# Kernel tuning notes

Measured on AMD Instinct MI355X. Metric: run time of the kernel, lower is better.

## Reference

```python
import jax, jax.numpy as jnp
import numpy as np

N_QUBITS = 8
TRASH = 1
DEPTH = 2
DIM = 2 ** N_QUBITS  # 256

# Qiskit little-endian: amplitude index k has qubit 0 as LSB. Reshaping a
# 256-vector to (2,)*8 puts qubit (N-1-a) on tensor axis a (axis 0 = MSB).
# Observable j is SparsePauliOp with 'Z' at string pos j => Z on qubit N-1-j
# => tensor axis j. So exp_j = sum probs * (1 - 2*bit_axis_j).


def _rx(t):
    c = jnp.cos(t / 2).astype(jnp.complex64)
    ms = (-1j * jnp.sin(t / 2)).astype(jnp.complex64)
    return jnp.stack([jnp.stack([c, ms]), jnp.stack([ms, c])])


def _ry(t):
    c = jnp.cos(t / 2).astype(jnp.complex64)
    s = jnp.sin(t / 2).astype(jnp.complex64)
    return jnp.stack([jnp.stack([c, -s]), jnp.stack([s, c])])


def _rz(t):
    e = jnp.exp((-0.5j) * t.astype(jnp.complex64))
    z = jnp.zeros_like(e)
    return jnp.stack([jnp.stack([e, z]), jnp.stack([z, jnp.conj(e)])])


def _apply_1q(psi, U, q):
    ax = 1 + (N_QUBITS - 1 - q)
    return jnp.moveaxis(jnp.tensordot(psi, U, axes=([ax], [1])), -1, ax)


def _apply_cx(psi, c, t):
    axc = 1 + (N_QUBITS - 1 - c)
    axt = 1 + (N_QUBITS - 1 - t)
    shape = [1] * psi.ndim
    shape[axc] = 2
    ctrl = (jnp.arange(2).reshape(shape) == 1)
    return jnp.where(ctrl, jnp.flip(psi, axis=axt), psi)


def _r3_ansatz(psi, theta, nq, depth):
    k = 0
    for _ in range(depth):
        for q in range(nq):
            psi = _apply_1q(psi, _rx(theta[k + 0]), q)
            psi = _apply_1q(psi, _ry(theta[k + 1]), q)
            psi = _apply_1q(psi, _rz(theta[k + 2]), q)
            k += 3
        for q in range(nq - 1):  # linear entanglement
            psi = _apply_cx(psi, q, q + 1)
    return psi


# sign matrix for Z expectations: S[j, k] = 1 - 2*bit_{N-1-j}(k)
_k = np.arange(DIM)
_SIGNS = np.stack([1.0 - 2.0 * ((_k >> (N_QUBITS - 1 - j)) & 1)
                   for j in range(N_QUBITS)]).astype(np.float32)  # (8, 256)


def setup_inputs() -> dict:
    key = jax.random.key(0)
    k1, k2, k3, k4 = jax.random.split(key, 4)
    return {
        "x": jax.random.normal(k1, (32, 1024, 256), dtype=jnp.float32),
        "theta1": jax.random.normal(k2, (DEPTH * N_QUBITS * 3,), dtype=jnp.float32),
        "theta2": jax.random.normal(k3, (DEPTH * (N_QUBITS - TRASH) * 3,), dtype=jnp.float32),
        "theta3": jax.random.normal(k4, (DEPTH * N_QUBITS * 3,), dtype=jnp.float32),
    }


def reference(x, theta1, theta2, theta3):
    B, T, D = x.shape
    xf = x.reshape(B * T, D)
    # amplitude encode: normalize classical vector into quantum amplitudes
    norm = jnp.linalg.norm(xf, axis=1, keepdims=True)
    norm = jnp.where(norm == 0, jnp.float32(1e-8), norm)
    psi = (xf / norm).astype(jnp.complex64).reshape((B * T,) + (2,) * N_QUBITS)
    # ansatz: U1 (8q) -> U2 (7q) -> U3 (8q)
    psi = _r3_ansatz(psi, theta1, N_QUBITS, DEPTH)
    psi = _r3_ansatz(psi, theta2, N_QUBITS - TRASH, DEPTH)
    psi = _r3_ansatz(psi, theta3, N_QUBITS, DEPTH)
    # Z expectation on each observable
    probs = (jnp.abs(psi) ** 2).reshape(B * T, DIM)
    y = probs @ jnp.asarray(_SIGNS).T  # (B*T, 8)
    # amplitude decode: normalize, |.|^2, zero-pad to DIM
    yn = jnp.linalg.norm(y, axis=1, keepdims=True)
    yn = jnp.where(yn == 0, jnp.float32(1e-8), yn)
    cv = (y / yn) ** 2
    out = jnp.pad(cv, ((0, 0), (0, DIM - N_QUBITS)))
    return out.reshape(B, T, DIM)
```

## Files before the change

kernel.cpp:

```cpp
#include <hip/hip_runtime.h>
#include <math.h>


#define DEV __device__ __forceinline__

typedef __attribute__((ext_vector_type(8))) short short8;
typedef __attribute__((ext_vector_type(4))) float f32x4;

DEV float2 cmul(float2 a, float2 b) {
  return make_float2(a.x * b.x - a.y * b.y, a.x * b.y + a.y * b.x);
}
DEV float2 cadd(float2 a, float2 b) { return make_float2(a.x + b.x, a.y + b.y); }

DEV unsigned short bf_rne(float v) {
  unsigned u = __float_as_uint(v);
  return (unsigned short)((u + 0x7FFFu + ((u >> 16) & 1u)) >> 16);
}

template <int CTRL>
DEV float dppf(float v) {
  return __int_as_float(__builtin_amdgcn_mov_dpp(__float_as_int(v), CTRL, 0xF, 0xF, true));
}
DEV float px1(float v) { return dppf<0xB1>(v); }
DEV float px2(float v) { return dppf<0x4E>(v); }
DEV float px4(float v) { return dppf<0x1B>(dppf<0x141>(v)); }
DEV float px8(float v) { return dppf<0x141>(dppf<0x140>(v)); }
DEV float fsgn(float v, int m) { return __int_as_float(__float_as_int(v) ^ m); }


struct Psi4 { float re[4]; float im[4]; };

template <int Q>
DEV void pair_gate(Psi4& s, const float2* __restrict__ Mlo,
                   const float2* __restrict__ Mhi, int lane) {
  const int b0 = (lane >> Q) & 1, b1 = (lane >> (Q + 1)) & 1;
  float2 lo_d = Mlo[b0 * 2 + b0];
  float2 lo_o = Mlo[b0 * 2 + (b0 ^ 1)];
  float2 hi_d = Mhi[b1 * 2 + b1];
  float2 hi_o = Mhi[b1 * 2 + (b1 ^ 1)];
  float2 c00 = cmul(hi_d, lo_d);
  float2 c01 = cmul(hi_d, lo_o);
  float2 c10 = cmul(hi_o, lo_d);
  float2 c11 = cmul(hi_o, lo_o);
  const int m0 = 1 << Q, m1 = 2 << Q;
#pragma unroll
  for (int r = 0; r < 4; ++r) {
    float ar = s.re[r], ai = s.im[r];
    float p0r = __shfl_xor(ar, m0, 64), p0i = __shfl_xor(ai, m0, 64);
    float p1r = __shfl_xor(ar, m1, 64), p1i = __shfl_xor(ai, m1, 64);
    float p2r = __shfl_xor(ar, m0 | m1, 64), p2i = __shfl_xor(ai, m0 | m1, 64);
    float nr = c00.x * ar - c00.y * ai + c01.x * p0r - c01.y * p0i
             + c10.x * p1r - c10.y * p1i + c11.x * p2r - c11.y * p2i;
    float ni = c00.x * ai + c00.y * ar + c01.x * p0i + c01.y * p0r
             + c10.x * p1i + c10.y * p1r + c11.x * p2i + c11.y * p2r;
    s.re[r] = nr; s.im[r] = ni;
  }
}

DEV void regpair_gate(Psi4& s, const float2* __restrict__ Mlo,
                      const float2* __restrict__ Mhi) {
  float nr[4], ni[4];
#pragma unroll
  for (int r = 0; r < 4; ++r) {
    const int b0 = r & 1, b1 = (r >> 1) & 1;
    float2 c00 = cmul(Mhi[b1 * 2 + b1], Mlo[b0 * 2 + b0]);
    float2 c01 = cmul(Mhi[b1 * 2 + b1], Mlo[b0 * 2 + (b0 ^ 1)]);
    float2 c10 = cmul(Mhi[b1 * 2 + (b1 ^ 1)], Mlo[b0 * 2 + b0]);
    float2 c11 = cmul(Mhi[b1 * 2 + (b1 ^ 1)], Mlo[b0 * 2 + (b0 ^ 1)]);
    nr[r] = c00.x * s.re[r] - c00.y * s.im[r]
          + c01.x * s.re[r ^ 1] - c01.y * s.im[r ^ 1]
          + c10.x * s.re[r ^ 2] - c10.y * s.im[r ^ 2]
          + c11.x * s.re[r ^ 3] - c11.y * s.im[r ^ 3];
    ni[r] = c00.x * s.im[r] + c00.y * s.re[r]
          + c01.x * s.im[r ^ 1] + c01.y * s.re[r ^ 1]
          + c10.x * s.im[r ^ 2] + c10.y * s.re[r ^ 2]
          + c11.x * s.im[r ^ 3] + c11.y * s.re[r ^ 3];
  }
#pragma unroll
  for (int r = 0; r < 4; ++r) { s.re[r] = nr[r]; s.im[r] = ni[r]; }
}

DEV void reg0_gate(Psi4& s, const float2* __restrict__ M) {
  float nr[4], ni[4];
#pragma unroll
  for (int r = 0; r < 4; ++r) {
    const int b = r & 1;
    float2 d = M[b * 2 + b], o = M[b * 2 + (b ^ 1)];
    nr[r] = d.x * s.re[r] - d.y * s.im[r] + o.x * s.re[r ^ 1] - o.y * s.im[r ^ 1];
    ni[r] = d.x * s.im[r] + d.y * s.re[r] + o.x * s.im[r ^ 1] + o.y * s.re[r ^ 1];
  }
#pragma unroll
  for (int r = 0; r < 4; ++r) { s.re[r] = nr[r]; s.im[r] = ni[r]; }
}

template <bool FULL8>
DEV void perm_cx(Psi4& s, int lane) {
  const int slane = (lane ^ (lane << 1)) & 63;
  const bool L5 = ((lane >> 5) & 1) != 0;
  float nr[4], ni[4];
#pragma unroll
  for (int r = 0; r < 4; ++r) {
    const int r0 = r & 1, r1 = (r >> 1) & 1;
    const int hiBit = FULL8 ? (r1 ^ r0) : r1;
    const int sA = (hiBit << 1) | r0;
    const int sB = sA ^ 1;
    float aRe = __shfl(s.re[sA], slane, 64);
    float aIm = __shfl(s.im[sA], slane, 64);
    float bRe = __shfl(s.re[sB], slane, 64);
    float bIm = __shfl(s.im[sB], slane, 64);
    nr[r] = L5 ? bRe : aRe;
    ni[r] = L5 ? bIm : aIm;
  }
#pragma unroll
  for (int r = 0; r < 4; ++r) { s.re[r] = nr[r]; s.im[r] = ni[r]; }
}

template <int NQ>
DEV void ansatz_f(Psi4& s, const float2* __restrict__ Mg, int lane) {
#pragma unroll
  for (int d = 0; d < 2; ++d) {
    const float2* Md = Mg + d * NQ * 4;
    pair_gate<0>(s, Md + 0, Md + 4, lane);
    pair_gate<2>(s, Md + 8, Md + 12, lane);
    pair_gate<4>(s, Md + 16, Md + 20, lane);
    if (NQ == 8) regpair_gate(s, Md + 24, Md + 28);
    else reg0_gate(s, Md + 24);
    perm_cx<NQ == 8>(s, lane);
  }
}

DEV void store_v(unsigned short* __restrict__ Vsw, int n, int kk, float v) {
  int k = kk >> 5, rem = kk & 31, quad = rem >> 3, jj = rem & 7;
  int nn = n & 255;
  int w = (nn >> 6) & 3, t = (nn >> 4) & 3, cl = nn & 15;
  int g = w * 8 + ((n >= 256) ? 4 + t : t);
  int L = quad * 16 + cl;
  size_t base = (size_t)k * 16384 + (size_t)g * 512 + (size_t)L * 8 + jj;
  Vsw[base] = bf_rne(v);
}

__global__ void build_u(const float* __restrict__ th1, const float* __restrict__ th2,
                        const float* __restrict__ th3, unsigned short* __restrict__ Vsw) {
  __shared__ float2 Mg[46 * 4];
  const int tid = threadIdx.x;
  if (tid < 46) {
    float thx, thy, thz;
    if (tid < 16)      { thx = th1[tid * 3]; thy = th1[tid * 3 + 1]; thz = th1[tid * 3 + 2]; }
    else if (tid < 30) { int u = (tid - 16) * 3; thx = th2[u]; thy = th2[u + 1]; thz = th2[u + 2]; }
    else               { int u = (tid - 30) * 3; thx = th3[u]; thy = th3[u + 1]; thz = th3[u + 2]; }
    float sx, cx_, sy, cy_, sz, cz_;
    sincosf(0.5f * thx, &sx, &cx_);
    sincosf(0.5f * thy, &sy, &cy_);
    sincosf(0.5f * thz, &sz, &cz_);
    float2 rx[4] = {{cx_, 0}, {0, -sx}, {0, -sx}, {cx_, 0}};
    float2 ry[4] = {{cy_, 0}, {-sy, 0}, {sy, 0}, {cy_, 0}};
    float2 A0 = cadd(cmul(ry[0], rx[0]), cmul(ry[1], rx[2]));
    float2 A1 = cadd(cmul(ry[0], rx[1]), cmul(ry[1], rx[3]));
    float2 A2 = cadd(cmul(ry[2], rx[0]), cmul(ry[3], rx[2]));
    float2 A3 = cadd(cmul(ry[2], rx[1]), cmul(ry[3], rx[3]));
    float2 ezm = make_float2(cz_, -sz), ezp = make_float2(cz_, sz);
    Mg[tid * 4 + 0] = cmul(ezm, A0);
    Mg[tid * 4 + 1] = cmul(ezm, A1);
    Mg[tid * 4 + 2] = cmul(ezp, A2);
    Mg[tid * 4 + 3] = cmul(ezp, A3);
  }
  __syncthreads();

  const int lane = tid & 63;
  const int j = blockIdx.x * 4 + (tid >> 6);
  Psi4 s;
#pragma unroll
  for (int r = 0; r < 4; ++r) {
    int a = (r << 6) | lane;
    s.re[r] = (a == j) ? 1.f : 0.f;
    s.im[r] = 0.f;
  }
  ansatz_f<8>(s, Mg, lane);
  ansatz_f<7>(s, Mg + 16 * 4, lane);
  ansatz_f<8>(s, Mg + 30 * 4, lane);
#pragma unroll
  for (int r = 0; r < 4; ++r) {
    int a = (r << 6) | lane;
    store_v(Vsw, a, j, s.re[r]);
    store_v(Vsw, a + 256, j, s.im[r]);
  }
}


__global__ __launch_bounds__(512, 4) void pqc_main(const float* __restrict__ x,
                                                   const unsigned short* __restrict__ Vsw,
                                                   float* __restrict__ out) {
  const int tid = threadIdx.x;
  const int ww = tid >> 6;
  const int w = ww >> 1;
  const int half = ww & 1;
  const int L = tid & 63;
  const int quad = L >> 4;
  const int c = L & 15;
  const int row0 = blockIdx.x * 64;

  __shared__ unsigned short A2[8][4][512];
  __shared__ float ys[64][8];
  __shared__ float invn[64];
  float* part = (float*)&A2[0][0][0];

  {
    const float4* xsrc = (const float4*)(x + (size_t)row0 * 256);
    const int r8 = L & 7;
    const int kf = L >> 3;
    const int q = kf >> 1;
    const int jj0 = (kf & 1) * 4;
#pragma unroll
    for (int i = 0; i < 8; ++i) {
      int row = i * 8 + r8;
      float4 f = xsrc[row * 64 + ww * 8 + kf];
      ushort4 h;
      h.x = bf_rne(f.x); h.y = bf_rne(f.y); h.z = bf_rne(f.z); h.w = bf_rne(f.w);
      int mt = row >> 4, cc = row & 15;
      int idx = (q * 16 + (cc ^ (q << 1))) * 8 + jj0;
      *(ushort4*)&A2[ww][mt][idx] = h;
    }
  }
  __syncthreads();

  f32x4 acc[4][4];
#pragma unroll
  for (int mt = 0; mt < 4; ++mt)
#pragma unroll
    for (int tt = 0; tt < 4; ++tt) acc[mt][tt] = (f32x4){0.f, 0.f, 0.f, 0.f};

  const unsigned short* pb = Vsw + (size_t)w * 4096 + (size_t)half * 2048 + (size_t)L * 8;
  const int sL8 = (quad * 16 + (c ^ (quad << 1))) * 8;

#pragma unroll 1
  for (int k = 0; k < 8; ++k) {
    short8 ah[4];
#pragma unroll
    for (int mt = 0; mt < 4; ++mt)
      ah[mt] = *(const short8*)&A2[k][mt][sL8];
    const unsigned short* pk = pb + (size_t)k * 16384;
#pragma unroll
    for (int tt = 0; tt < 4; ++tt) {
      short8 bh = *(const short8*)(pk + tt * 512);
#pragma unroll
      for (int mt = 0; mt < 4; ++mt)
        acc[mt][tt] = __builtin_amdgcn_mfma_f32_16x16x32_bf16(ah[mt], bh, acc[mt][tt], 0, 0, 0);
    }
  }
  __syncthreads();

  const int m1 = (c & 1) << 31;
  const int m2 = (c & 2) << 30;
  const int m4 = (c & 4) << 29;
  const int m8 = (c & 8) << 28;
#pragma unroll
  for (int mt = 0; mt < 4; ++mt) {
#pragma unroll
    for (int r = 0; r < 4; ++r) {
      float p0 = acc[mt][0][r] * acc[mt][0][r];
      float p1 = acc[mt][1][r] * acc[mt][1][r];
      float p2 = acc[mt][2][r] * acc[mt][2][r];
      float p3 = acc[mt][3][r] * acc[mt][3][r];
      float s01 = p0 + p1, s23 = p2 + p3;
      float av = s01 + s23;
      float bv = s01 - s23;
      float cv = (p0 - p1) + (p2 - p3);
      av = px1(av) + fsgn(av, m1);
      bv += px1(bv);  cv += px1(cv);
      av = px2(av) + fsgn(av, m2);
      bv += px2(bv);  cv += px2(cv);
      av = px4(av) + fsgn(av, m4);
      bv += px4(bv);  cv += px4(cv);
      av = px8(av) + fsgn(av, m8);
      bv += px8(bv);  cv += px8(cv);
      int m = mt * 16 + quad * 4 + r;
      float* pm = part + (ww * 64 + m) * 8;
      if (c == 0) {
        pm[0] = ((w >> 1) & 1) ? -av : av;
        pm[1] = (w & 1) ? -av : av;
        pm[2] = bv;
        pm[3] = cv;
      } else if (c == 8) pm[4] = av;
      else if (c == 4) pm[5] = av;
      else if (c == 2) pm[6] = av;
      else if (c == 1) pm[7] = av;
    }
  }
  __syncthreads();

  {
    int m = tid >> 3, jj = tid & 7;
    float acc_y = 0.f;
#pragma unroll
    for (int p = 0; p < 8; ++p) acc_y += part[(p * 64 + m) * 8 + jj];
    ys[m][jj] = acc_y;
  }
  __syncthreads();

  if (tid < 64) {
    float n = 0.f;
#pragma unroll
    for (int jj = 0; jj < 8; ++jj) { float v = ys[tid][jj]; n = fmaf(v, v, n); }
    n = sqrtf(n);
    invn[tid] = (n == 0.f) ? 0.f : 1.f / n;
  }
  __syncthreads();

  float4* o4 = (float4*)(out + (size_t)row0 * 256);
#pragma unroll
  for (int i = 0; i < 8; ++i) {
    int e = i * 512 + tid;
    int row = e >> 6;
    int c4 = (e & 63) * 4;
    float4 v = make_float4(0.f, 0.f, 0.f, 0.f);
    if (c4 < 8) {
      float iv = invn[row];
      float t0 = ys[row][c4 + 0] * iv;
      float t1 = ys[row][c4 + 1] * iv;
      float t2 = ys[row][c4 + 2] * iv;
      float t3 = ys[row][c4 + 3] * iv;
      v = make_float4(t0 * t0, t1 * t1, t2 * t2, t3 * t3);
    }
    o4[e] = v;
  }
}

extern "C" void kernel_launch(void* const* d_in, const int* in_sizes, int n_in,
                              void* d_out, int out_size, void* d_ws, size_t ws_size,
                              hipStream_t stream) {
  const float* x = (const float*)d_in[0];
  const float* th1 = (const float*)d_in[1];
  const float* th2 = (const float*)d_in[2];
  const float* th3 = (const float*)d_in[3];
  float* out = (float*)d_out;
  unsigned short* Vsw = (unsigned short*)d_ws;

  build_u<<<64, 256, 0, stream>>>(th1, th2, th3, Vsw);
  pqc_main<<<512, 512, 0, stream>>>(x, Vsw, out);
}
```

Measured before the change: 108.9 us.

## Switch MFMA to fp16, software-prefetch B fragments, fuse norm reduction via DPP

Changes the matrix operand precision from bf16 to fp16 (both the state and the unitary), using the f16 MFMA. Restructures the K loop to prefetch the next iteration's B fragments into registers while MFMAs run, hiding global load latency. Also replaces a separate barrier plus serial row-norm step with a DPP butterfly reduction inside the partial-sum step, removing one __syncthreads. fp16 has narrower range, but normalized amplitudes fit, and it gives more mantissa precision.

```diff
diff --git a/kernel.cpp b/kernel.cpp
--- a/kernel.cpp
+++ b/kernel.cpp
@@ -4,7 +4,7 @@
 
 #define DEV __device__ __forceinline__
 
-typedef __attribute__((ext_vector_type(8))) short short8;
+typedef __attribute__((ext_vector_type(8))) _Float16 half8;
 typedef __attribute__((ext_vector_type(4))) float f32x4;
 
 DEV float2 cmul(float2 a, float2 b) {
@@ -12,9 +12,9 @@
 }
 DEV float2 cadd(float2 a, float2 b) { return make_float2(a.x + b.x, a.y + b.y); }
 
-DEV unsigned short bf_rne(float v) {
-  unsigned u = __float_as_uint(v);
-  return (unsigned short)((u + 0x7FFFu + ((u >> 16) & 1u)) >> 16);
+DEV unsigned short f16b(float v) {
+  _Float16 h = (_Float16)v;
+  return __builtin_bit_cast(unsigned short, h);
 }
 
 template <int CTRL>
@@ -136,7 +136,7 @@
   int g = w * 8 + ((n >= 256) ? 4 + t : t);
   int L = quad * 16 + cl;
   size_t base = (size_t)k * 16384 + (size_t)g * 512 + (size_t)L * 8 + jj;
-  Vsw[base] = bf_rne(v);
+  Vsw[base] = f16b(v);
 }
 
 __global__ void build_u(const float* __restrict__ th1, const float* __restrict__ th2,
@@ -204,6 +204,11 @@
   __shared__ float invn[64];
   float* part = (float*)&A2[0][0][0];
 
+  const unsigned short* pb = Vsw + (size_t)w * 4096 + (size_t)half * 2048 + (size_t)L * 8;
+
+  half8 b0 = *(const half8*)(pb);
+  half8 b1 = *(const half8*)(pb + 512);
+
   {
     const float4* xsrc = (const float4*)(x + (size_t)row0 * 256);
     const int r8 = L & 7;
@@ -215,7 +220,7 @@
       int row = i * 8 + r8;
       float4 f = xsrc[row * 64 + ww * 8 + kf];
       ushort4 h;
-      h.x = bf_rne(f.x); h.y = bf_rne(f.y); h.z = bf_rne(f.z); h.w = bf_rne(f.w);
+      h.x = f16b(f.x); h.y = f16b(f.y); h.z = f16b(f.z); h.w = f16b(f.w);
       int mt = row >> 4, cc = row & 15;
       int idx = (q * 16 + (cc ^ (q << 1))) * 8 + jj0;
       *(ushort4*)&A2[ww][mt][idx] = h;
@@ -229,23 +234,33 @@
 #pragma unroll
     for (int tt = 0; tt < 4; ++tt) acc[mt][tt] = (f32x4){0.f, 0.f, 0.f, 0.f};
 
-  const unsigned short* pb = Vsw + (size_t)w * 4096 + (size_t)half * 2048 + (size_t)L * 8;
   const int sL8 = (quad * 16 + (c ^ (quad << 1))) * 8;
 
 #pragma unroll 1
   for (int k = 0; k < 8; ++k) {
-    short8 ah[4];
-#pragma unroll
-    for (int mt = 0; mt < 4; ++mt)
-      ah[mt] = *(const short8*)&A2[k][mt][sL8];
+    half8 ah[4];
+#pragma unroll
+    for (int mt = 0; mt < 4; ++mt)
+      ah[mt] = *(const half8*)&A2[k][mt][sL8];
     const unsigned short* pk = pb + (size_t)k * 16384;
-#pragma unroll
-    for (int tt = 0; tt < 4; ++tt) {
-      short8 bh = *(const short8*)(pk + tt * 512);
-#pragma unroll
-      for (int mt = 0; mt < 4; ++mt)
-        acc[mt][tt] = __builtin_amdgcn_mfma_f32_16x16x32_bf16(ah[mt], bh, acc[mt][tt], 0, 0, 0);
-    }
+    const unsigned short* pn = pb + (size_t)((k < 7) ? k + 1 : k) * 16384;
+
+    half8 b2 = *(const half8*)(pk + 2 * 512);
+#pragma unroll
+    for (int mt = 0; mt < 4; ++mt)
+      acc[mt][0] = __builtin_amdgcn_mfma_f32_16x16x32_f16(ah[mt], b0, acc[mt][0], 0, 0, 0);
+    half8 b3 = *(const half8*)(pk + 3 * 512);
+#pragma unroll
+    for (int mt = 0; mt < 4; ++mt)
+      acc[mt][1] = __builtin_amdgcn_mfma_f32_16x16x32_f16(ah[mt], b1, acc[mt][1], 0, 0, 0);
+    b0 = *(const half8*)(pn);
+#pragma unroll
+    for (int mt = 0; mt < 4; ++mt)
+      acc[mt][2] = __builtin_amdgcn_mfma_f32_16x16x32_f16(ah[mt], b2, acc[mt][2], 0, 0, 0);
+    b1 = *(const half8*)(pn + 512);
+#pragma unroll
+    for (int mt = 0; mt < 4; ++mt)
+      acc[mt][3] = __builtin_amdgcn_mfma_f32_16x16x32_f16(ah[mt], b3, acc[mt][3], 0, 0, 0);
   }
   __syncthreads();
 
@@ -294,15 +309,11 @@
 #pragma unroll
     for (int p = 0; p < 8; ++p) acc_y += part[(p * 64 + m) * 8 + jj];
     ys[m][jj] = acc_y;
-  }
-  __syncthreads();
-
-  if (tid < 64) {
-    float n = 0.f;
-#pragma unroll
-    for (int jj = 0; jj < 8; ++jj) { float v = ys[tid][jj]; n = fmaf(v, v, n); }
-    n = sqrtf(n);
-    invn[tid] = (n == 0.f) ? 0.f : 1.f / n;
+    float sq = acc_y * acc_y;
+    sq += px1(sq);
+    sq += px2(sq);
+    sq += px4(sq);
+    if (jj == 0) invn[m] = (sq == 0.f) ? 0.f : 1.f / sqrtf(sq);
   }
   __syncthreads();
 
```

After: 108.8 us. About the same (-0.0%).
